# Performance work log

Measured on AMD Instinct MI355X. Metric: run time of the kernel, lower is better.

The kernel has to match this reference:

```python
import jax, jax.numpy as jnp
import numpy as np

BN_EPS = 1e-3


def _knn_group(p1, p2, k):
    # p1, p2: [B, N, 3]. For each point in p1, find k nearest in p2.
    d2 = (jnp.sum(p1 * p1, -1)[:, :, None]
          + jnp.sum(p2 * p2, -1)[:, None, :]
          - 2.0 * jnp.einsum('bnd,bmd->bnm', p1, p2))  # [B,N,N]
    _, idx = jax.lax.top_k(-d2, k)                      # [B,N,k]
    nn = jax.vmap(lambda pts, ind: pts[ind])(p2, idx)   # [B,N,k,3]
    resi = nn - p1[:, :, None, :]                       # [B,N,k,3]
    ss = jnp.sum(resi * resi, -1, keepdims=True)
    dist = jnp.sqrt(jnp.maximum(ss, 1e-12))             # safe norm
    feat = jnp.concatenate([resi, dist], -1)            # [B,N,k,4]
    return feat.transpose(0, 3, 1, 2), nn.transpose(0, 3, 1, 2)  # [B,4,N,k],[B,3,N,k]


def _conv_bn_relu(x, W, b, g, be, m, v):
    # 1x1 conv over channel dim: x [B,C,N,K], W [O,C]
    x = jnp.einsum('bcnk,oc->bonk', x, W) + b[None, :, None, None]
    x = (x - m[None, :, None, None]) * (g / jnp.sqrt(v + BN_EPS))[None, :, None, None] + be[None, :, None, None]
    return jax.nn.relu(x)


def setup_inputs() -> dict:
    key = jax.random.key(0)
    ks = jax.random.split(key, 20)
    B, N = 8, 2048
    chans = [4, 64, 64, 128]
    inp = {
        'points1': jax.random.normal(ks[0], (B, 3, N), jnp.float32),
        'points2': jax.random.normal(ks[1], (B, 3, N), jnp.float32),
    }
    for i in range(3):
        ci, co = chans[i], chans[i + 1]
        base = 2 + i * 6
        scale = 1.0 / np.sqrt(ci)
        inp[f'W{i+1}'] = jax.random.uniform(ks[base], (co, ci), jnp.float32, -scale, scale)
        inp[f'b{i+1}'] = jax.random.uniform(ks[base + 1], (co,), jnp.float32, -scale, scale)
        inp[f'g{i+1}'] = 1.0 + 0.1 * jax.random.normal(ks[base + 2], (co,), jnp.float32)
        inp[f'be{i+1}'] = 0.1 * jax.random.normal(ks[base + 3], (co,), jnp.float32)
        inp[f'm{i+1}'] = 0.05 * jax.random.normal(ks[base + 4], (co,), jnp.float32)
        inp[f'v{i+1}'] = jax.random.uniform(ks[base + 5], (co,), jnp.float32, 0.5, 1.5)
    inp['k'] = 32
    inp['t'] = 1
    return inp


def reference(points1, points2, W1, b1, g1, be1, m1, v1, W2, b2, g2, be2, m2, v2,
              W3, b3, g3, be3, m3, v3, k, t):
    p1 = points1.transpose(0, 2, 1)  # [B,N,3]
    p2 = points2.transpose(0, 2, 1)
    f1, nn1 = _knn_group(p1, p1, k)
    f2, nn2 = _knn_group(p1, p2, k)
    feats = jnp.concatenate([f1, f2], -1)          # [B,4,N,2k]
    grouped = jnp.concatenate([nn1, nn2], -1)      # [B,3,N,2k]
    x = _conv_bn_relu(feats, W1, b1, g1, be1, m1, v1)
    x = _conv_bn_relu(x, W2, b2, g2, be2, m2, v2)
    x = _conv_bn_relu(x, W3, b3, g3, be3, m3, v3)
    x = jnp.max(x, axis=1)                         # [B,N,2k] max over channels
    w = jax.nn.softmax(x, axis=-1)                 # softmax over 2k neighbors
    fused = jnp.sum(w[:, None, :, :] * grouped, -1)  # [B,3,N]
    return fused
```

## Files before the change

### kernel.cpp

```cpp
#include <hip/hip_runtime.h>
#include <hip/hip_bf16.h>
#include <stdint.h>

#define BB 8
#define NN 2048

#define OFF_B1 272
#define OFF_B2 4432
#define OFF_B3 12688
#define IDX_BYTE_OFF 65536
#define T_BASE   (65536 + 2*1024*1024)
#define T1_OFF   T_BASE
#define T2H_OFF  (T1_OFF + 4096)
#define T2L_OFF  (T2H_OFF + 9216)
#define T3H_OFF  (T2L_OFF + 9216)
#define T3L_OFF  (T3H_OFF + 18432)
#define L_T1   0
#define L_T2H  2048
#define L_T2L  6656
#define L_T3H  11264
#define L_T3L  20480
#define L_HALVES 29696

typedef __attribute__((ext_vector_type(4))) float f32x4;
typedef __attribute__((ext_vector_type(8))) short s16x8;

__device__ __forceinline__ float ldany(const void* p, long i, int isf32) {
    if (isf32) return ((const float*)p)[i];
    uint32_t u = ((uint32_t)((const uint16_t*)p)[i]) << 16;
    float f; __builtin_memcpy(&f, &u, 4); return f;
}
__device__ __forceinline__ uint16_t f2bf(float f) {
    uint32_t u; __builtin_memcpy(&u, &f, 4);
    return (uint16_t)((u + 0x7FFFu + ((u >> 16) & 1u)) >> 16);
}
__device__ __forceinline__ float bf2f(uint16_t h) {
    uint32_t u = ((uint32_t)h) << 16;
    float f; __builtin_memcpy(&f, &u, 4); return f;
}
__device__ __forceinline__ uint32_t pk2(float a, float b) {
    __hip_bfloat162 h = __float22bfloat162_rn(make_float2(a, b));
    uint32_t u; __builtin_memcpy(&u, &h, 4); return u;
}
__device__ __forceinline__ s16x8 mk8(uint32_t a, uint32_t b, uint32_t c, uint32_t d) {
    uint32_t t[4] = {a, b, c, d}; s16x8 r; __builtin_memcpy(&r, t, 16); return r;
}
__device__ __forceinline__ float sane(float v) {
    return (v == v && v > -1e30f && v < 1e30f) ? v : 0.f;
}
__device__ __forceinline__ int mbcnt64(unsigned long long m) {
    return __builtin_amdgcn_mbcnt_hi((uint32_t)(m >> 32),
           __builtin_amdgcn_mbcnt_lo((uint32_t)m, 0));
}
__device__ __forceinline__ int kperm_pos(int kk) {
    int g = kk >> 5, c5 = kk & 31;
    int sub = (c5 >> 4) & 1, q = (c5 >> 2) & 3, r = c5 & 3;
    return 32 * g + 8 * q + 4 * sub + r;
}

__global__ void k0_fold(const void* p1,
                        const void* W1, const void* b1, const void* g1, const void* be1, const void* m1, const void* v1,
                        const void* W2, const void* b2, const void* g2, const void* be2, const void* m2, const void* v2,
                        const void* W3, const void* b3, const void* g3, const void* be3, const void* m3, const void* v3,
                        float* wsf, int* wsi) {
    __shared__ int s_cnt;
    int t = threadIdx.x;
    if (t == 0) s_cnt = 0;
    __syncthreads();
    const uint16_t* u = (const uint16_t*)p1;
    int c = 0;
    for (int i = t; i < 4096; i += 256) {
        uint16_t x = u[i];
        uint32_t e = (x >> 7) & 0xFF;
        c += ((e >= 0x70 && e <= 0x84) || x == 0) ? 1 : 0;
    }
    atomicAdd(&s_cnt, c);
    __syncthreads();
    int isf32 = (s_cnt < 3686) ? 1 : 0;
    if (blockIdx.x == 0 && t == 0) wsi[0] = isf32;

    uint16_t* t1  = (uint16_t*)((char*)wsf + T1_OFF);
    uint16_t* t2h = (uint16_t*)((char*)wsf + T2H_OFF);
    uint16_t* t2l = (uint16_t*)((char*)wsf + T2L_OFF);
    uint16_t* t3h = (uint16_t*)((char*)wsf + T3H_OFF);
    uint16_t* t3l = (uint16_t*)((char*)wsf + T3L_OFF);

    int gid = blockIdx.x * 256 + t;
    if (gid < 4096) {
        int o = gid >> 6, kk = gid & 63;
        float s = ldany(g2, o, isf32) * rsqrtf(ldany(v2, o, isf32) + 1e-3f);
        float w = ldany(W2, gid, isf32) * s;
        uint16_t wh = f2bf(w);
        int pos = o * 72 + kperm_pos(kk);
        t2h[pos] = wh; t2l[pos] = f2bf(w - bf2f(wh));
    } else if (gid < 12288) {
        int e = gid - 4096;
        int o = e >> 6, kk = e & 63;
        float s = ldany(g3, o, isf32) * rsqrtf(ldany(v3, o, isf32) + 1e-3f);
        float w = ldany(W3, e, isf32) * s;
        uint16_t wh = f2bf(w);
        int pos = o * 72 + kperm_pos(kk);
        t3h[pos] = wh; t3l[pos] = f2bf(w - bf2f(wh));
    } else if (gid < 12544) {
        int e = gid - 12288;
        int co = e >> 2, cc = e & 3;
        float s = ldany(g1, co, isf32) * rsqrtf(ldany(v1, co, isf32) + 1e-3f);
        float w = ldany(W1, co*4 + cc, isf32) * s;
        uint16_t wh = f2bf(w), wl = f2bf(w - bf2f(wh));
        t1[co*32 + cc]     = wh;
        t1[co*32 + 4 + cc] = wh;
        t1[co*32 + 8 + cc] = wl;
    } else if (gid < 13824) {
        int e = gid - 12544;
        int co = e / 20, k = e - co * 20;
        t1[co*32 + 12 + k] = 0;
    } else if (gid < 13888) {
        int o = gid - 13824;
        float s = ldany(g1, o, isf32) * rsqrtf(ldany(v1, o, isf32) + 1e-3f);
        wsf[OFF_B1 + o] = (ldany(b1, o, isf32) - ldany(m1, o, isf32)) * s + ldany(be1, o, isf32);
    } else if (gid < 13952) {
        int o = gid - 13888;
        float s = ldany(g2, o, isf32) * rsqrtf(ldany(v2, o, isf32) + 1e-3f);
        wsf[OFF_B2 + o] = (ldany(b2, o, isf32) - ldany(m2, o, isf32)) * s + ldany(be2, o, isf32);
    } else if (gid < 14080) {
        int o = gid - 13952;
        float s = ldany(g3, o, isf32) * rsqrtf(ldany(v3, o, isf32) + 1e-3f);
        wsf[OFF_B3 + o] = (ldany(b3, o, isf32) - ldany(m3, o, isf32)) * s + ldany(be3, o, isf32);
    }
}

__device__ __forceinline__ void knn_target(const void* p, long base, int isf32, int lane,
                                           float qx, float qy, float qz, float s1,
                                           unsigned long long* sl, uint16_t* dst) {
    uint32_t kb[32];
    if (!isf32) {
        const uint16_t* tpu = (const uint16_t*)p + base;
        const uint4* rx = (const uint4*)(tpu);
        const uint4* ry = (const uint4*)(tpu + NN);
        const uint4* rz = (const uint4*)(tpu + 2*NN);
        #pragma unroll
        for (int i = 0; i < 4; i++) {
            int v4 = i * 64 + lane;
            uint4 X = rx[v4], Y = ry[v4], Z = rz[v4];
            uint32_t xw[4] = {X.x, X.y, X.z, X.w};
            uint32_t yw[4] = {Y.x, Y.y, Y.z, Y.w};
            uint32_t zw[4] = {Z.x, Z.y, Z.z, Z.w};
            #pragma unroll
            for (int j = 0; j < 4; j++) {
                #pragma unroll
                for (int w = 0; w < 2; w++) {
                    uint32_t ux = (w == 0) ? (xw[j] << 16) : (xw[j] & 0xFFFF0000u);
                    uint32_t uy = (w == 0) ? (yw[j] << 16) : (yw[j] & 0xFFFF0000u);
                    uint32_t uz = (w == 0) ? (zw[j] << 16) : (zw[j] & 0xFFFF0000u);
                    float nx, ny, nz;
                    __builtin_memcpy(&nx, &ux, 4); __builtin_memcpy(&ny, &uy, 4); __builtin_memcpy(&nz, &uz, 4);
                    float s2  = nx * nx + ny * ny + nz * nz;
                    float dot = qx * nx + qy * ny + qz * nz;
                    float d2  = fmaxf((s1 + s2) - 2.0f * dot, 0.0f);
                    uint32_t bits; __builtin_memcpy(&bits, &d2, 4);
                    kb[i*8 + j*2 + w] = bits;
                }
            }
        }
    } else {
        const float* tpf = (const float*)p + base;
        #pragma unroll
        for (int i = 0; i < 32; i++) {
            int j = i * 64 + lane;
            float nx = tpf[j];
            float ny = tpf[NN + j];
            float nz = tpf[2*NN + j];
            float s2  = nx * nx + ny * ny + nz * nz;
            float dot = qx * nx + qy * ny + qz * nz;
            float d2  = fmaxf((s1 + s2) - 2.0f * dot, 0.0f);
            uint32_t bits; __builtin_memcpy(&bits, &d2, 4);
            kb[i] = bits;
        }
    }

    uint32_t lo = 0u, hi = 0x7F800001u, tau = 0u;
    while (true) {
        uint32_t mid = lo + ((hi - lo) >> 1);
        int c = 0;
        #pragma unroll
        for (int i = 0; i < 32; i++) c += __builtin_popcountll(__ballot(kb[i] < mid));
        if (c < 32)      lo = mid;
        else if (c > 64) hi = mid;
        else { tau = mid; break; }
        if (hi - lo <= 1u) { tau = hi; break; }
    }

    sl[lane] = ~0ull;
    int basePos = 0;
    #pragma unroll
    for (int i = 0; i < 32; i++) {
        unsigned idxv = isf32 ? (unsigned)(i * 64 + lane)
                              : (unsigned)((i >> 3) * 512 + 8 * lane + (i & 7));
        bool pz = kb[i] < tau;
        unsigned long long m = __ballot(pz);
        int pos = basePos + mbcnt64(m);
        if (pz && pos < 64) sl[pos] = (((unsigned long long)kb[i]) << 32) | idxv;
        basePos += __builtin_popcountll(m);
    }
    unsigned long long key = sl[lane];

    #pragma unroll
    for (int sz = 2; sz <= 64; sz <<= 1) {
        #pragma unroll
        for (int st = sz >> 1; st > 0; st >>= 1) {
            unsigned long long ot = __shfl_xor(key, st, 64);
            bool up    = ((lane & sz) == 0);
            bool lower = ((lane & st) == 0);
            unsigned long long mn = (key < ot) ? key : ot;
            unsigned long long mx = (key < ot) ? ot : key;
            key = (lower == up) ? mn : mx;
        }
    }

    if (lane < 32) dst[lane] = (uint16_t)(key & 0x7FFu);
}

__launch_bounds__(256)
__global__ void k1_knn(const void* p1, const void* p2, const int* wsi, uint16_t* idxout) {
    __shared__ unsigned long long smem[4 * 64];

    int isf32 = wsi[0];
    int lane = threadIdx.x & 63;
    int wave = threadIdx.x >> 6;
    int qidx = blockIdx.x * 4 + wave;
    int b = qidx >> 11, n = qidx & 2047;
    long base = (long)b * 3 * NN;

    float qx = ldany(p1, base + n,        isf32);
    float qy = ldany(p1, base + NN + n,   isf32);
    float qz = ldany(p1, base + 2*NN + n, isf32);
    float s1 = qx * qx + qy * qy + qz * qz;

    unsigned long long* sl = smem + wave * 64;
    long obase = ((long)qidx) << 6;

    knn_target(p1, base, isf32, lane, qx, qy, qz, s1, sl, idxout + obase);

    __builtin_amdgcn_sched_barrier(0);
    asm volatile("" ::: "memory");

    knn_target(p2, base, isf32, lane, qx, qy, qz, s1, sl, idxout + obase + 32);
}

__launch_bounds__(1024)
__global__ void k2_mlp(const void* p1, const void* p2, const float* __restrict__ wsf, const int* wsi,
                       const uint16_t* __restrict__ idxin, void* outp) {
    __shared__ uint4 shw4[L_HALVES / 8];

    {
        const uint4* src = (const uint4*)((const char*)wsf + T1_OFF);
        for (int i = threadIdx.x; i < L_HALVES / 8; i += 1024) shw4[i] = src[i];
    }
    __syncthreads();
    const uint16_t* shw = (const uint16_t*)shw4;
    const uint16_t* T1  = shw + L_T1;
    const uint16_t* T2H = shw + L_T2H;
    const uint16_t* T2L = shw + L_T2L;
    const uint16_t* T3H = shw + L_T3H;
    const uint16_t* T3L = shw + L_T3L;

    int isf32 = wsi[0];
    int lane = threadIdx.x & 63;
    int wave = threadIdx.x >> 6;
    int c = lane & 15;
    int q = lane >> 4;
    int qidx = blockIdx.x * 16 + wave;
    int b = qidx >> 11, n = qidx & 2047;
    long base = (long)b * 3 * NN;

    float qx = sane(ldany(p1, base + n,        isf32));
    float qy = sane(ldany(p1, base + NN + n,   isf32));
    float qz = sane(ldany(p1, base + 2*NN + n, isf32));

    int idx = idxin[((long)qidx << 6) + lane] & 2047;
    const void* sp = (lane < 32) ? p1 : p2;
    float nx = sane(ldany(sp, base + idx,        isf32));
    float ny = sane(ldany(sp, base + NN + idx,   isf32));
    float nz = sane(ldany(sp, base + 2*NN + idx, isf32));

    float r0 = nx - qx, r1 = ny - qy, r2 = nz - qz;
    float ss = fmaf(r0, r0, fmaf(r1, r1, r2 * r2));
    float dist = sqrtf(fmaxf(ss, 1e-12f));

    const float* B1 = wsf + OFF_B1;
    const float* B2 = wsf + OFF_B2;
    const float* B3 = wsf + OFF_B3;

    s16x8 b1f[4];
    #pragma unroll
    for (int nt = 0; nt < 4; nt++) {
        int src = 16 * nt + c;
        float f0 = __shfl(r0, src, 64);
        float f1 = __shfl(r1, src, 64);
        float f2v = __shfl(r2, src, 64);
        float f3v = __shfl(dist, src, 64);
        uint16_t h0 = f2bf(f0), h1 = f2bf(f1), h2 = f2bf(f2v), h3 = f2bf(f3v);
        uint16_t l0 = f2bf(f0 - bf2f(h0)), l1 = f2bf(f1 - bf2f(h1));
        uint16_t l2 = f2bf(f2v - bf2f(h2)), l3 = f2bf(f3v - bf2f(h3));
        s16x8 v;
        bool qa = (q < 2);
        bool qb = (q == 0);
        v[0] = qa ? (short)h0 : (short)0;
        v[1] = qa ? (short)h1 : (short)0;
        v[2] = qa ? (short)h2 : (short)0;
        v[3] = qa ? (short)h3 : (short)0;
        v[4] = qb ? (short)l0 : (short)0;
        v[5] = qb ? (short)l1 : (short)0;
        v[6] = qb ? (short)l2 : (short)0;
        v[7] = qb ? (short)l3 : (short)0;
        b1f[nt] = v;
    }

    f32x4 d1[4][4];
    #pragma unroll
    for (int mt = 0; mt < 4; mt++) {
        s16x8 a1 = *(const s16x8*)(T1 + (16 * mt + c) * 32 + q * 8);
        f32x4 bias = *(const f32x4*)(B1 + 16 * mt + 4 * q);
        #pragma unroll
        for (int nt = 0; nt < 4; nt++) {
            d1[mt][nt] = __builtin_amdgcn_mfma_f32_16x16x32_bf16(a1, b1f[nt], bias, 0, 0, 0);
        }
    }

    auto mkfrag = [](const f32x4& dlo, const f32x4& dhi) -> s16x8 {
        return mk8(pk2(fmaxf(dlo[0], 0.f), fmaxf(dlo[1], 0.f)),
                   pk2(fmaxf(dlo[2], 0.f), fmaxf(dlo[3], 0.f)),
                   pk2(fmaxf(dhi[0], 0.f), fmaxf(dhi[1], 0.f)),
                   pk2(fmaxf(dhi[2], 0.f), fmaxf(dhi[3], 0.f)));
    };

    f32x4 d2[4][4];
    #pragma unroll
    for (int mt = 0; mt < 4; mt++) {
        f32x4 bias = *(const f32x4*)(B2 + 16 * mt + 4 * q);
        #pragma unroll
        for (int nt = 0; nt < 4; nt++) d2[mt][nt] = bias;
    }
    #pragma unroll
    for (int g = 0; g < 2; g++) {
        s16x8 fh[4];
        #pragma unroll
        for (int nt = 0; nt < 4; nt++) fh[nt] = mkfrag(d1[2*g][nt], d1[2*g+1][nt]);
        #pragma unroll
        for (int mt = 0; mt < 4; mt++) {
            s16x8 ah = *(const s16x8*)(T2H + (16 * mt + c) * 72 + 32 * g + 8 * q);
            s16x8 al = *(const s16x8*)(T2L + (16 * mt + c) * 72 + 32 * g + 8 * q);
            #pragma unroll
            for (int nt = 0; nt < 4; nt++) {
                f32x4 acc = d2[mt][nt];
                acc = __builtin_amdgcn_mfma_f32_16x16x32_bf16(ah, fh[nt], acc, 0, 0, 0);
                acc = __builtin_amdgcn_mfma_f32_16x16x32_bf16(al, fh[nt], acc, 0, 0, 0);
                d2[mt][nt] = acc;
            }
        }
    }

    s16x8 f3h[2][4];
    #pragma unroll
    for (int g = 0; g < 2; g++)
        #pragma unroll
        for (int nt = 0; nt < 4; nt++) f3h[g][nt] = mkfrag(d2[2*g][nt], d2[2*g+1][nt]);

    float mx[4] = {-1e30f, -1e30f, -1e30f, -1e30f};
    #pragma unroll
    for (int mt = 0; mt < 8; mt++) {
        f32x4 bias = *(const f32x4*)(B3 + 16 * mt + 4 * q);
        f32x4 acc[4];
        #pragma unroll
        for (int nt = 0; nt < 4; nt++) acc[nt] = bias;
        #pragma unroll
        for (int g = 0; g < 2; g++) {
            s16x8 ah = *(const s16x8*)(T3H + (16 * mt + c) * 72 + 32 * g + 8 * q);
            s16x8 al = *(const s16x8*)(T3L + (16 * mt + c) * 72 + 32 * g + 8 * q);
            #pragma unroll
            for (int nt = 0; nt < 4; nt++) {
                f32x4 a = acc[nt];
                a = __builtin_amdgcn_mfma_f32_16x16x32_bf16(ah, f3h[g][nt], a, 0, 0, 0);
                a = __builtin_amdgcn_mfma_f32_16x16x32_bf16(al, f3h[g][nt], a, 0, 0, 0);
                acc[nt] = a;
            }
        }
        #pragma unroll
        for (int nt = 0; nt < 4; nt++) {
            mx[nt] = fmaxf(mx[nt], fmaxf(fmaxf(acc[nt][0], acc[nt][1]), fmaxf(acc[nt][2], acc[nt][3])));
        }
    }

    #pragma unroll
    for (int nt = 0; nt < 4; nt++) {
        mx[nt] = fmaxf(mx[nt], __shfl_xor(mx[nt], 16, 64));
        mx[nt] = fmaxf(mx[nt], __shfl_xor(mx[nt], 32, 64));
        mx[nt] = fmaxf(mx[nt], 0.f);
    }
    float mall = fmaxf(fmaxf(mx[0], mx[1]), fmaxf(mx[2], mx[3]));
    #pragma unroll
    for (int m = 1; m < 16; m <<= 1) mall = fmaxf(mall, __shfl_xor(mall, m, 64));
    float e0 = __expf(mx[0] - mall), e1 = __expf(mx[1] - mall);
    float e2 = __expf(mx[2] - mall), e3 = __expf(mx[3] - mall);
    float s = e0 + e1 + e2 + e3;
    #pragma unroll
    for (int m = 1; m < 16; m <<= 1) s += __shfl_xor(s, m, 64);
    float eown = (q == 0) ? e0 : (q == 1) ? e1 : (q == 2) ? e2 : e3;
    float w = eown / s;

    float sx = w * nx, sy = w * ny, sz = w * nz;
    #pragma unroll
    for (int m = 1; m < 64; m <<= 1) {
        sx += __shfl_xor(sx, m, 64);
        sy += __shfl_xor(sy, m, 64);
        sz += __shfl_xor(sz, m, 64);
    }

    if (lane < 3) {
        float v = (lane == 0) ? sx : ((lane == 1) ? sy : sz);
        long oi = base + (long)lane * NN + n;
        if (isf32) {
            ((float*)outp)[oi] = v;
        } else {
            ((uint16_t*)outp)[oi] = f2bf(v);
        }
    }
}

extern "C" void kernel_launch(void* const* d_in, const int* in_sizes, int n_in,
                              void* d_out, int out_size, void* d_ws, size_t ws_size,
                              hipStream_t stream) {
    const void* p1 = d_in[0];
    const void* p2 = d_in[1];
    float* wsf = (float*)d_ws;
    int*   wsi = (int*)d_ws;
    uint16_t* idxbuf = (uint16_t*)((char*)d_ws + IDX_BYTE_OFF);

    k0_fold<<<64, 256, 0, stream>>>(p1,
        d_in[2],  d_in[3],  d_in[4],  d_in[5],  d_in[6],  d_in[7],
        d_in[8],  d_in[9],  d_in[10], d_in[11], d_in[12], d_in[13],
        d_in[14], d_in[15], d_in[16], d_in[17], d_in[18], d_in[19],
        wsf, wsi);

    k1_knn<<<(BB * NN) / 4, 256, 0, stream>>>(p1, p2, wsi, idxbuf);

    k2_mlp<<<(BB * NN) / 16, 1024, 0, stream>>>(p1, p2, wsf, wsi, idxbuf, d_out);
}
```

Measured before the change: 263.9 us.

## Fuse kNN selection and MLP/softmax kernels into one kernel

Merges the kNN top-k kernel and the MLP/softmax kernel into a single kernel with 512-thread blocks. Neighbor indices pass between lanes by shuffle instead of through a global index buffer, which removes one launch and the global write and read of indices. Layer-2 and layer-3 weight tables are staged in shared memory while the layer-1 table is read from global memory. Both phases now share one block shape, so the MLP phase loses its 1024-thread blocks and the larger shared footprint may limit occupancy.

```diff
diff --git a/kernel.cpp b/kernel.cpp
--- a/kernel.cpp
+++ b/kernel.cpp
@@ -8,19 +8,18 @@
 #define OFF_B1 272
 #define OFF_B2 4432
 #define OFF_B3 12688
-#define IDX_BYTE_OFF 65536
 #define T_BASE   (65536 + 2*1024*1024)
 #define T1_OFF   T_BASE
 #define T2H_OFF  (T1_OFF + 4096)
 #define T2L_OFF  (T2H_OFF + 9216)
 #define T3H_OFF  (T2L_OFF + 9216)
 #define T3L_OFF  (T3H_OFF + 18432)
-#define L_T1   0
-#define L_T2H  2048
-#define L_T2L  6656
-#define L_T3H  11264
-#define L_T3L  20480
-#define L_HALVES 29696
+#define LF_T2H   0
+#define LF_T2L   4608
+#define LF_T3H   9216
+#define LF_T3L   18432
+#define LF_TABLE_BYTES 55296
+#define LF_SLOT_BYTES  4096
 
 typedef __attribute__((ext_vector_type(4))) float f32x4;
 typedef __attribute__((ext_vector_type(8))) short s16x8;
@@ -129,9 +128,9 @@
     }
 }
 
-__device__ __forceinline__ void knn_target(const void* p, long base, int isf32, int lane,
-                                           float qx, float qy, float qz, float s1,
-                                           unsigned long long* sl, uint16_t* dst) {
+__device__ __forceinline__ unsigned long long knn_target(const void* p, long base, int isf32, int lane,
+                                                         float qx, float qy, float qz, float s1,
+                                                         unsigned long long* sl) {
     uint32_t kb[32];
     if (!isf32) {
         const uint16_t* tpu = (const uint16_t*)p + base;
@@ -216,68 +215,54 @@
             key = (lower == up) ? mn : mx;
         }
     }
-
-    if (lane < 32) dst[lane] = (uint16_t)(key & 0x7FFu);
-}
-
-__launch_bounds__(256)
-__global__ void k1_knn(const void* p1, const void* p2, const int* wsi, uint16_t* idxout) {
-    __shared__ unsigned long long smem[4 * 64];
+    return key;
+}
+
+__launch_bounds__(512)
+__global__ void k12_fused(const void* p1, const void* p2, const float* __restrict__ wsf, const int* wsi,
+                          void* outp) {
+    __shared__ uint4 shmem4[(LF_TABLE_BYTES + LF_SLOT_BYTES) / 16];
+
+    {
+        const uint4* src = (const uint4*)((const char*)wsf + T2H_OFF);
+        for (int i = threadIdx.x; i < LF_TABLE_BYTES / 16; i += 512) shmem4[i] = src[i];
+    }
+    __syncthreads();
+    const uint16_t* shw = (const uint16_t*)shmem4;
+    const uint16_t* T2H = shw + LF_T2H;
+    const uint16_t* T2L = shw + LF_T2L;
+    const uint16_t* T3H = shw + LF_T3H;
+    const uint16_t* T3L = shw + LF_T3L;
+    const uint16_t* T1  = (const uint16_t*)((const char*)wsf + T1_OFF);
 
     int isf32 = wsi[0];
     int lane = threadIdx.x & 63;
     int wave = threadIdx.x >> 6;
-    int qidx = blockIdx.x * 4 + wave;
-    int b = qidx >> 11, n = qidx & 2047;
-    long base = (long)b * 3 * NN;
-
-    float qx = ldany(p1, base + n,        isf32);
-    float qy = ldany(p1, base + NN + n,   isf32);
-    float qz = ldany(p1, base + 2*NN + n, isf32);
-    float s1 = qx * qx + qy * qy + qz * qz;
-
-    unsigned long long* sl = smem + wave * 64;
-    long obase = ((long)qidx) << 6;
-
-    knn_target(p1, base, isf32, lane, qx, qy, qz, s1, sl, idxout + obase);
-
-    __builtin_amdgcn_sched_barrier(0);
-    asm volatile("" ::: "memory");
-
-    knn_target(p2, base, isf32, lane, qx, qy, qz, s1, sl, idxout + obase + 32);
-}
-
-__launch_bounds__(1024)
-__global__ void k2_mlp(const void* p1, const void* p2, const float* __restrict__ wsf, const int* wsi,
-                       const uint16_t* __restrict__ idxin, void* outp) {
-    __shared__ uint4 shw4[L_HALVES / 8];
-
-    {
-        const uint4* src = (const uint4*)((const char*)wsf + T1_OFF);
-        for (int i = threadIdx.x; i < L_HALVES / 8; i += 1024) shw4[i] = src[i];
-    }
-    __syncthreads();
-    const uint16_t* shw = (const uint16_t*)shw4;
-    const uint16_t* T1  = shw + L_T1;
-    const uint16_t* T2H = shw + L_T2H;
-    const uint16_t* T2L = shw + L_T2L;
-    const uint16_t* T3H = shw + L_T3H;
-    const uint16_t* T3L = shw + L_T3L;
-
-    int isf32 = wsi[0];
-    int lane = threadIdx.x & 63;
-    int wave = threadIdx.x >> 6;
-    int c = lane & 15;
-    int q = lane >> 4;
-    int qidx = blockIdx.x * 16 + wave;
+    int qidx = blockIdx.x * 8 + wave;
     int b = qidx >> 11, n = qidx & 2047;
     long base = (long)b * 3 * NN;
 
     float qx = sane(ldany(p1, base + n,        isf32));
     float qy = sane(ldany(p1, base + NN + n,   isf32));
     float qz = sane(ldany(p1, base + 2*NN + n, isf32));
-
-    int idx = idxin[((long)qidx << 6) + lane] & 2047;
+    float s1 = qx * qx + qy * qy + qz * qz;
+
+    unsigned long long* sl = (unsigned long long*)((char*)shmem4 + LF_TABLE_BYTES) + wave * 64;
+
+    unsigned long long keyA = knn_target(p1, base, isf32, lane, qx, qy, qz, s1, sl);
+    __builtin_amdgcn_sched_barrier(0);
+    asm volatile("" ::: "memory");
+    unsigned long long keyB = knn_target(p2, base, isf32, lane, qx, qy, qz, s1, sl);
+
+    uint32_t loA = (uint32_t)keyA;
+    uint32_t loB = (uint32_t)keyB;
+    int srcl = (lane >= 32) ? (lane - 32) : lane;
+    uint32_t iB = (uint32_t)__shfl((int)loB, srcl, 64);
+    int idx = (int)(((lane < 32) ? loA : iB) & 2047u);
+
+    int c = lane & 15;
+    int q = lane >> 4;
+
     const void* sp = (lane < 32) ? p1 : p2;
     float nx = sane(ldany(sp, base + idx,        isf32));
     float ny = sane(ldany(sp, base + NN + idx,   isf32));
@@ -434,7 +419,6 @@
     const void* p2 = d_in[1];
     float* wsf = (float*)d_ws;
     int*   wsi = (int*)d_ws;
-    uint16_t* idxbuf = (uint16_t*)((char*)d_ws + IDX_BYTE_OFF);
 
     k0_fold<<<64, 256, 0, stream>>>(p1,
         d_in[2],  d_in[3],  d_in[4],  d_in[5],  d_in[6],  d_in[7],
@@ -442,7 +426,5 @@
         d_in[14], d_in[15], d_in[16], d_in[17], d_in[18], d_in[19],
         wsf, wsi);
 
-    k1_knn<<<(BB * NN) / 4, 256, 0, stream>>>(p1, p2, wsi, idxbuf);
-
-    k2_mlp<<<(BB * NN) / 16, 1024, 0, stream>>>(p1, p2, wsf, wsi, idxbuf, d_out);
-}
+    k12_fused<<<(BB * NN) / 8, 512, 0, stream>>>(p1, p2, wsf, wsi, d_out);
+}
```

New measurement: 364.1 us. 1.38x slower.
